# Kernel tuning notes

Hardware: AMD Instinct MI355X
Metric: run time of the kernel (lower is better)

## Reference

```python
import jax, jax.numpy as jnp
import numpy as np

P = 512       # input_shape
HD = 256      # hidden_dim
N = 65536     # number of samples
LAM1 = 1.0
LAM3 = 1.0


def setup_inputs() -> dict:
    key = jax.random.key(0)
    ks = jax.random.split(key, 12)
    def lin(kw, kb, out_d, in_d):
        lim = 1.0 / np.sqrt(in_d)
        W = jax.random.uniform(kw, (out_d, in_d), jnp.float32, -lim, lim)
        b = jax.random.uniform(kb, (out_d,), jnp.float32, -lim, lim)
        return W, b
    W1, b1 = lin(ks[0], ks[1], 200, P + HD)
    W12, b12 = lin(ks[2], ks[3], 100, 200)
    W13, b13 = lin(ks[4], ks[5], 100, 100)
    W2, b2 = lin(ks[6], ks[7], P, 100)
    return {
        "input": jax.random.normal(ks[8], (N, P), jnp.float32),
        "h": jax.random.normal(ks[9], (N, HD), jnp.float32),
        "W1": W1, "b1": b1, "W12": W12, "b12": b12,
        "W13": W13, "b13": b13, "W2": W2, "b2": b2,
        "idx0": 0, "idx1": N,
    }


def reference(input, h, W1, b1, W12, b12, W13, b13, W2, b2, idx0, idx1):
    n = input.shape[0]
    hs = h[idx0:idx1]                                   # [N, HD]
    x = jnp.concatenate([input, hs], axis=1)            # [N, P+HD]
    x = jax.nn.relu(x @ W1.T + b1)                      # dropout = identity (eval)
    x = jax.nn.relu(x @ W12.T + b12)
    x = jax.nn.relu(x @ W13.T + b13)
    f_x_h = x @ W2.T + b2                               # [N, P]
    mu = jnp.mean(hs, axis=0)                           # [HD]
    # S = mean_i <h_i, h_i> : vectorized sum-of-squares (replaces Python loop)
    S = jnp.mean(jnp.sum(hs * hs, axis=1))
    part0 = jnp.linalg.norm(f_x_h[:-1] - input[1:]) / (n - 1)
    part1 = LAM1 * jnp.sum(jnp.abs(mu)) / HD
    part2 = LAM1 * jnp.abs(S / HD - 1.0)
    part3 = LAM3 * jnp.mean(jnp.sum(jnp.abs(hs[1:] - hs[:-1]), axis=1)) / HD
    return (f_x_h, part0, part1, part2, part3)
```

## Files before the change

kernel.cpp:

```cpp
#include <hip/hip_runtime.h>

typedef __bf16 bf16;
typedef __bf16 bf16x8 __attribute__((ext_vector_type(8)));
typedef float f32x4 __attribute__((ext_vector_type(4)));

#define N_ROWS 65536

#define W1P_E  (208 * 768)
#define W12P_E (112 * 224)
#define W13P_E (112 * 128)
#define W2P_E  (512 * 128)
#define WP_TOTAL (W1P_E + W12P_E + W13P_E + W2P_E)
#define BP_OFF_BYTES (WP_TOTAL * 2)
#define BP_FLOATS 944
#define ACC_OFF_BYTES (BP_OFF_BYTES + BP_FLOATS * 4)
#define ACC_FLOATS 259

__global__ void pack_kernel(const float* __restrict__ W1, const float* __restrict__ b1,
                            const float* __restrict__ W12, const float* __restrict__ b12,
                            const float* __restrict__ W13, const float* __restrict__ b13,
                            const float* __restrict__ W2, const float* __restrict__ b2,
                            bf16* __restrict__ wp, float* __restrict__ bp) {
  int i = blockIdx.x * 256 + threadIdx.x;
  if (i < WP_TOTAL) {
    float v = 0.0f;
    if (i < W1P_E) {
      int o = i / 768, k = i - o * 768;
      if (o < 200) v = W1[o * 768 + k];
    } else if (i < W1P_E + W12P_E) {
      int j = i - W1P_E;
      int o = j / 224, k = j - o * 224;
      if (o < 100 && k < 200) v = W12[o * 200 + k];
    } else if (i < W1P_E + W12P_E + W13P_E) {
      int j = i - (W1P_E + W12P_E);
      int o = j / 128, k = j - o * 128;
      if (o < 100 && k < 100) v = W13[o * 100 + k];
    } else {
      int j = i - (W1P_E + W12P_E + W13P_E);
      int o = j / 128, k = j - o * 128;
      if (k < 100) v = W2[o * 100 + k];
    }
    wp[i] = (bf16)v;
  } else {
    int j = i - WP_TOTAL;
    if (j < BP_FLOATS) {
      float v = 0.0f;
      if (j < 208)      { if (j < 200) v = b1[j]; }
      else if (j < 320) { int o = j - 208; if (o < 100) v = b12[o]; }
      else if (j < 432) { int o = j - 320; if (o < 100) v = b13[o]; }
      else              { v = b2[j - 432]; }
      bp[j] = v;
    }
  }
}

__device__ inline bf16x8 cvt8(const float* __restrict__ p) {
  f32x4 lo = *(const f32x4*)p;
  f32x4 hi = *(const f32x4*)(p + 4);
  bf16x8 r;
#pragma unroll
  for (int i = 0; i < 4; i++) { r[i] = (bf16)lo[i]; r[4 + i] = (bf16)hi[i]; }
  return r;
}

#define MFMA(a, b, c) __builtin_amdgcn_mfma_f32_16x16x32_bf16((a), (b), (c), 0, 0, 0)

template<int ITERS, int R, int SRC_STRIDE>
__device__ inline void stage_load(bf16x8* r, const bf16* __restrict__ src, int k0, int tid) {
#pragma unroll
  for (int i = 0; i < ITERS; i++) {
    int e = tid + i * 256;
    if (ITERS * 256 == R * 4 || e < R * 4) {
      int row = e >> 2, seg = e & 3;
      r[i] = *(const bf16x8*)(src + (size_t)row * SRC_STRIDE + k0 + seg * 8);
    }
  }
}
template<int ITERS, int R>
__device__ inline void stage_write(bf16* dst, const bf16x8* r, int tid) {
#pragma unroll
  for (int i = 0; i < ITERS; i++) {
    int e = tid + i * 256;
    if (ITERS * 256 == R * 4 || e < R * 4) {
      int row = e >> 2, seg = e & 3;
      int ps = seg ^ ((row ^ (row >> 2)) & 3);
      *(bf16x8*)(dst + row * 32 + ps * 8) = r[i];
    }
  }
}

__global__ __launch_bounds__(256, 4) void mlp_main(
    const float* __restrict__ input, const float* __restrict__ h,
    const bf16* __restrict__ wp, const float* __restrict__ bp,
    float* __restrict__ out, float* __restrict__ p0_accum) {
  __shared__ __align__(16) bf16 acts[4][3712];
  __shared__ __align__(16) bf16 wbuf[2][6656];

  const int tid = threadIdx.x;
  const int lane = tid & 63;
  const int wave = tid >> 6;
  const int c16 = lane & 15;
  const int quad = lane >> 4;
  const int m0 = blockIdx.x * 64 + wave * 16;
  const int qs8 = (quad ^ ((c16 ^ (c16 >> 2)) & 3)) * 8;

  const bf16* W1p  = wp;
  const bf16* W12p = wp + W1P_E;
  const bf16* W13p = wp + W1P_E + W12P_E;
  const bf16* W2p  = wp + W1P_E + W12P_E + W13P_E;
  const float* b1p  = bp;
  const float* b12p = bp + 208;
  const float* b13p = bp + 320;
  const float* b2p  = bp + 432;

  bf16* actw = &acts[wave][0];
  bf16x8 sreg[4];

  f32x4 acc1[13];
#pragma unroll
  for (int t = 0; t < 13; t++) acc1[t] = (f32x4){0.f, 0.f, 0.f, 0.f};

  stage_load<4, 208, 768>(sreg, W1p, 0, tid);
  stage_write<4, 208>(wbuf[0], sreg, tid);
  __syncthreads();

  const float* arow = input + (size_t)(m0 + c16) * 512;
  const float* hrow = h + (size_t)(m0 + c16) * 256;
  for (int ks = 0; ks < 24; ks++) {
    if (ks + 1 < 24) stage_load<4, 208, 768>(sreg, W1p, (ks + 1) * 32, tid);
    const int k0 = ks * 32;
    bf16x8 a = (k0 < 512) ? cvt8(arow + k0 + quad * 8) : cvt8(hrow + (k0 - 512) + quad * 8);
    const bf16* buf = wbuf[ks & 1];
#pragma unroll
    for (int t = 0; t < 13; t++) {
      bf16x8 b = *(const bf16x8*)(buf + (t * 16 + c16) * 32 + qs8);
      acc1[t] = MFMA(a, b, acc1[t]);
    }
    if (ks + 1 < 24) stage_write<4, 208>(wbuf[(ks + 1) & 1], sreg, tid);
    __syncthreads();
  }
#pragma unroll
  for (int t = 0; t < 13; t++) {
    const float bias = b1p[t * 16 + c16];
#pragma unroll
    for (int r = 0; r < 4; r++)
      actw[(quad * 4 + r) * 232 + t * 16 + c16] = (bf16)fmaxf(acc1[t][r] + bias, 0.0f);
  }
  for (int idx = lane; idx < 256; idx += 64)
    actw[(idx >> 4) * 232 + 208 + (idx & 15)] = (bf16)0.0f;

  f32x4 acc2[7];
#pragma unroll
  for (int t = 0; t < 7; t++) acc2[t] = (f32x4){0.f, 0.f, 0.f, 0.f};

  stage_load<2, 112, 224>(sreg, W12p, 0, tid);
  stage_write<2, 112>(wbuf[0], sreg, tid);
  __syncthreads();
  for (int ks = 0; ks < 7; ks++) {
    if (ks + 1 < 7) stage_load<2, 112, 224>(sreg, W12p, (ks + 1) * 32, tid);
    const int k0 = ks * 32;
    bf16x8 a = *(const bf16x8*)(actw + c16 * 232 + k0 + quad * 8);
    const bf16* buf = wbuf[ks & 1];
#pragma unroll
    for (int t = 0; t < 7; t++) {
      bf16x8 b = *(const bf16x8*)(buf + (t * 16 + c16) * 32 + qs8);
      acc2[t] = MFMA(a, b, acc2[t]);
    }
    if (ks + 1 < 7) stage_write<2, 112>(wbuf[(ks + 1) & 1], sreg, tid);
    __syncthreads();
  }
#pragma unroll
  for (int t = 0; t < 7; t++) {
    const float bias = b12p[t * 16 + c16];
#pragma unroll
    for (int r = 0; r < 4; r++)
      actw[(quad * 4 + r) * 136 + t * 16 + c16] = (bf16)fmaxf(acc2[t][r] + bias, 0.0f);
  }
  for (int idx = lane; idx < 256; idx += 64)
    actw[(idx >> 4) * 136 + 112 + (idx & 15)] = (bf16)0.0f;

  f32x4 acc3[7];
#pragma unroll
  for (int t = 0; t < 7; t++) acc3[t] = (f32x4){0.f, 0.f, 0.f, 0.f};

  stage_load<2, 112, 128>(sreg, W13p, 0, tid);
  stage_write<2, 112>(wbuf[0], sreg, tid);
  __syncthreads();
  for (int ks = 0; ks < 4; ks++) {
    if (ks + 1 < 4) stage_load<2, 112, 128>(sreg, W13p, (ks + 1) * 32, tid);
    const int k0 = ks * 32;
    bf16x8 a = *(const bf16x8*)(actw + c16 * 136 + k0 + quad * 8);
    const bf16* buf = wbuf[ks & 1];
#pragma unroll
    for (int t = 0; t < 7; t++) {
      bf16x8 b = *(const bf16x8*)(buf + (t * 16 + c16) * 32 + qs8);
      acc3[t] = MFMA(a, b, acc3[t]);
    }
    if (ks + 1 < 4) stage_write<2, 112>(wbuf[(ks + 1) & 1], sreg, tid);
    __syncthreads();
  }
#pragma unroll
  for (int t = 0; t < 7; t++) {
    const float bias = b13p[t * 16 + c16];
#pragma unroll
    for (int r = 0; r < 4; r++)
      actw[(quad * 4 + r) * 136 + t * 16 + c16] = (bf16)fmaxf(acc3[t][r] + bias, 0.0f);
  }
  for (int idx = lane; idx < 256; idx += 64)
    actw[(idx >> 4) * 136 + 112 + (idx & 15)] = (bf16)0.0f;

  float p0local = 0.0f;
  for (int g = 0; g < 4; g++) {
    f32x4 acc4[8];
#pragma unroll
    for (int t = 0; t < 8; t++) acc4[t] = (f32x4){0.f, 0.f, 0.f, 0.f};

    const bf16* Wg = W2p + (size_t)g * 128 * 128;
    stage_load<2, 128, 128>(sreg, Wg, 0, tid);
    stage_write<2, 128>(wbuf[0], sreg, tid);
    __syncthreads();
    for (int ks = 0; ks < 4; ks++) {
      if (ks + 1 < 4) stage_load<2, 128, 128>(sreg, Wg, (ks + 1) * 32, tid);
      const int k0 = ks * 32;
      bf16x8 a = *(const bf16x8*)(actw + c16 * 136 + k0 + quad * 8);
      const bf16* buf = wbuf[ks & 1];
#pragma unroll
      for (int t = 0; t < 8; t++) {
        bf16x8 b = *(const bf16x8*)(buf + (t * 16 + c16) * 32 + qs8);
        acc4[t] = MFMA(a, b, acc4[t]);
      }
      if (ks + 1 < 4) stage_write<2, 128>(wbuf[(ks + 1) & 1], sreg, tid);
      __syncthreads();
    }
#pragma unroll
    for (int t = 0; t < 8; t++) {
      const int o = g * 128 + t * 16 + c16;
      const float bias = b2p[o];
#pragma unroll
      for (int r = 0; r < 4; r++) {
        const int grow = m0 + quad * 4 + r;
        float v = acc4[t][r] + bias;
        out[(size_t)grow * 512 + o] = v;
        if (grow < N_ROWS - 1) {
          float d = v - input[(size_t)(grow + 1) * 512 + o];
          p0local += d * d;
        }
      }
    }
  }
#pragma unroll
  for (int off = 32; off > 0; off >>= 1) p0local += __shfl_down(p0local, off);
  if (lane == 0) atomicAdd(p0_accum, p0local);
}

__global__ __launch_bounds__(256) void reduce_h(const float* __restrict__ h, float* __restrict__ acc) {
  __shared__ f32x4 cbuf[256];
  __shared__ float redS[256];
  __shared__ float redP[256];
  const int t = threadIdx.x;
  const int c = t & 63;
  const int rg = t >> 6;
  const int start = blockIdx.x * 128 + rg * 32;

  const float* base = h + (size_t)start * 256 + c * 4;
  f32x4 prev = *(const f32x4*)base;
  f32x4 csum = prev;
  f32x4 s2v = prev * prev;
  f32x4 p3v = (f32x4){0.f, 0.f, 0.f, 0.f};
#pragma unroll 8
  for (int r = 1; r < 32; r++) {
    f32x4 v = *(const f32x4*)(base + (size_t)r * 256);
    csum += v;
    s2v += v * v;
    f32x4 d = v - prev;
#pragma unroll
    for (int i = 0; i < 4; i++) p3v[i] += __builtin_fabsf(d[i]);
    prev = v;
  }
  if (start + 32 < N_ROWS) {
    f32x4 v = *(const f32x4*)(base + (size_t)32 * 256);
    f32x4 d = v - prev;
#pragma unroll
    for (int i = 0; i < 4; i++) p3v[i] += __builtin_fabsf(d[i]);
  }
  cbuf[t] = csum;
  redS[t] = s2v[0] + s2v[1] + s2v[2] + s2v[3];
  redP[t] = p3v[0] + p3v[1] + p3v[2] + p3v[3];
  __syncthreads();
  if (rg == 0) {
    f32x4 s = cbuf[c] + cbuf[c + 64] + cbuf[c + 128] + cbuf[c + 192];
    atomicAdd(&acc[4 * c + 0], s[0]);
    atomicAdd(&acc[4 * c + 1], s[1]);
    atomicAdd(&acc[4 * c + 2], s[2]);
    atomicAdd(&acc[4 * c + 3], s[3]);
  }
  for (int s = 128; s > 0; s >>= 1) {
    if (t < s) { redS[t] += redS[t + s]; redP[t] += redP[t + s]; }
    __syncthreads();
  }
  if (t == 0) {
    atomicAdd(&acc[257], redS[0]);
    atomicAdd(&acc[258], redP[0]);
  }
}

__global__ void finalize(const float* __restrict__ acc, float* __restrict__ out) {
  __shared__ float red[256];
  const int t = threadIdx.x;
  red[t] = fabsf(acc[t]);
  __syncthreads();
  for (int s = 128; s > 0; s >>= 1) {
    if (t < s) red[t] += red[t + s];
    __syncthreads();
  }
  if (t == 0) {
    float part1 = red[0] / 65536.0f / 256.0f;
    float part0 = sqrtf(acc[256]) / 65535.0f;
    float part2 = fabsf(acc[257] / (65536.0f * 256.0f) - 1.0f);
    float part3 = acc[258] / (65535.0f * 256.0f);
    out[(size_t)N_ROWS * 512 + 0] = part0;
    out[(size_t)N_ROWS * 512 + 1] = part1;
    out[(size_t)N_ROWS * 512 + 2] = part2;
    out[(size_t)N_ROWS * 512 + 3] = part3;
  }
}

extern "C" void kernel_launch(void* const* d_in, const int* in_sizes, int n_in,
                              void* d_out, int out_size, void* d_ws, size_t ws_size,
                              hipStream_t stream) {
  const float* input = (const float*)d_in[0];
  const float* h   = (const float*)d_in[1];
  const float* W1  = (const float*)d_in[2];
  const float* b1  = (const float*)d_in[3];
  const float* W12 = (const float*)d_in[4];
  const float* b12 = (const float*)d_in[5];
  const float* W13 = (const float*)d_in[6];
  const float* b13 = (const float*)d_in[7];
  const float* W2  = (const float*)d_in[8];
  const float* b2  = (const float*)d_in[9];
  float* out = (float*)d_out;

  bf16* wp = (bf16*)d_ws;
  float* bp = (float*)((char*)d_ws + BP_OFF_BYTES);
  float* acc = (float*)((char*)d_ws + ACC_OFF_BYTES);

  hipMemsetAsync(acc, 0, ACC_FLOATS * sizeof(float), stream);
  pack_kernel<<<(WP_TOTAL + BP_FLOATS + 255) / 256, 256, 0, stream>>>(
      W1, b1, W12, b12, W13, b13, W2, b2, wp, bp);
  mlp_main<<<N_ROWS / 64, 256, 0, stream>>>(input, h, wp, bp, out, acc + 256);
  reduce_h<<<N_ROWS / 128, 256, 0, stream>>>(h, acc);
  finalize<<<1, 256, 0, stream>>>(acc, out);
}
```

Baseline: 490.4 us.

## Pre-swizzle weight tiles and stage via direct global-to-LDS loads; batch activation loads

The pack kernel now writes weights in per-k-step, pre-swizzled tile order, so the main kernel can copy each stage straight into LDS with global_load_lds and skip the register round trip. Layer-1 activation loads are batched eight k-steps at a time to expose more memory parallelism, and launch bounds drop from 4 to 2 blocks per SM. The p0 atomic is reduced per block first, and reduce_h uses fewer, larger blocks spreading the column sums over 16 accumulator copies to cut atomic contention. Risks include lower occupancy, higher register pressure from the activation buffer, and reliance on the asynchronous LDS copies being complete at the barrier.

```diff
diff --git a/kernel.cpp b/kernel.cpp
--- a/kernel.cpp
+++ b/kernel.cpp
@@ -6,15 +6,24 @@
 
 #define N_ROWS 65536
 
-#define W1P_E  (208 * 768)
-#define W12P_E (112 * 224)
-#define W13P_E (112 * 128)
-#define W2P_E  (512 * 128)
-#define WP_TOTAL (W1P_E + W12P_E + W13P_E + W2P_E)
+#define W1_E   159744
+#define W12_E  25088
+#define W13_E  14336
+#define W2_E   65536
+#define WP_TOTAL (W1_E + W12_E + W13_E + W2_E)
+#define W12_OFF_B 319488
+#define W13_OFF_B 369664
+#define W2_OFF_B  398336
 #define BP_OFF_BYTES (WP_TOTAL * 2)
 #define BP_FLOATS 944
 #define ACC_OFF_BYTES (BP_OFF_BYTES + BP_FLOATS * 4)
-#define ACC_FLOATS 259
+#define NCOPY 16
+#define ACC_FLOATS (NCOPY * 256 + 3)
+#define P0_IDX (NCOPY * 256)
+#define S_IDX  (NCOPY * 256 + 1)
+#define P3_IDX (NCOPY * 256 + 2)
+
+__device__ inline int swz4(int r) { return (r ^ (r >> 2)) & 3; }
 
 __global__ void pack_kernel(const float* __restrict__ W1, const float* __restrict__ b1,
                             const float* __restrict__ W12, const float* __restrict__ b12,
@@ -24,20 +33,30 @@
   int i = blockIdx.x * 256 + threadIdx.x;
   if (i < WP_TOTAL) {
     float v = 0.0f;
-    if (i < W1P_E) {
-      int o = i / 768, k = i - o * 768;
-      if (o < 200) v = W1[o * 768 + k];
-    } else if (i < W1P_E + W12P_E) {
-      int j = i - W1P_E;
-      int o = j / 224, k = j - o * 224;
-      if (o < 100 && k < 200) v = W12[o * 200 + k];
-    } else if (i < W1P_E + W12P_E + W13P_E) {
-      int j = i - (W1P_E + W12P_E);
-      int o = j / 128, k = j - o * 128;
-      if (o < 100 && k < 100) v = W13[o * 100 + k];
+    if (i < W1_E) {
+      int s = i / 6656, b = i - s * 6656;
+      int r = b >> 5, w = b & 31;
+      int k = s * 32 + (((w >> 3) ^ swz4(r)) << 3) + (w & 7);
+      if (r < 200) v = W1[r * 768 + k];
+    } else if (i < W1_E + W12_E) {
+      int j = i - W1_E;
+      int s = j / 3584, b = j - s * 3584;
+      int r = b >> 5, w = b & 31;
+      int k = s * 32 + (((w >> 3) ^ swz4(r)) << 3) + (w & 7);
+      if (r < 100 && k < 200) v = W12[r * 200 + k];
+    } else if (i < W1_E + W12_E + W13_E) {
+      int j = i - (W1_E + W12_E);
+      int s = j / 3584, b = j - s * 3584;
+      int r = b >> 5, w = b & 31;
+      int k = s * 32 + (((w >> 3) ^ swz4(r)) << 3) + (w & 7);
+      if (r < 100 && k < 100) v = W13[r * 100 + k];
     } else {
-      int j = i - (W1P_E + W12P_E + W13P_E);
-      int o = j / 128, k = j - o * 128;
+      int j = i - (W1_E + W12_E + W13_E);
+      int g = j >> 14, rest = j & 16383;
+      int s = rest >> 12, b = rest & 4095;
+      int r = b >> 5, w = b & 31;
+      int o = g * 128 + r;
+      int k = s * 32 + (((w >> 3) ^ swz4(r)) << 3) + (w & 7);
       if (k < 100) v = W2[o * 100 + k];
     }
     wp[i] = (bf16)v;
@@ -54,47 +73,31 @@
   }
 }
 
-__device__ inline bf16x8 cvt8(const float* __restrict__ p) {
-  f32x4 lo = *(const f32x4*)p;
-  f32x4 hi = *(const f32x4*)(p + 4);
-  bf16x8 r;
-#pragma unroll
-  for (int i = 0; i < 4; i++) { r[i] = (bf16)lo[i]; r[4 + i] = (bf16)hi[i]; }
-  return r;
-}
-
 #define MFMA(a, b, c) __builtin_amdgcn_mfma_f32_16x16x32_bf16((a), (b), (c), 0, 0, 0)
 
-template<int ITERS, int R, int SRC_STRIDE>
-__device__ inline void stage_load(bf16x8* r, const bf16* __restrict__ src, int k0, int tid) {
-#pragma unroll
-  for (int i = 0; i < ITERS; i++) {
-    int e = tid + i * 256;
-    if (ITERS * 256 == R * 4 || e < R * 4) {
-      int row = e >> 2, seg = e & 3;
-      r[i] = *(const bf16x8*)(src + (size_t)row * SRC_STRIDE + k0 + seg * 8);
-    }
-  }
-}
-template<int ITERS, int R>
-__device__ inline void stage_write(bf16* dst, const bf16x8* r, int tid) {
-#pragma unroll
-  for (int i = 0; i < ITERS; i++) {
-    int e = tid + i * 256;
-    if (ITERS * 256 == R * 4 || e < R * 4) {
-      int row = e >> 2, seg = e & 3;
-      int ps = seg ^ ((row ^ (row >> 2)) & 3);
-      *(bf16x8*)(dst + row * 32 + ps * 8) = r[i];
-    }
-  }
-}
-
-__global__ __launch_bounds__(256, 4) void mlp_main(
+template<int BYTES>
+__device__ inline void stage(const char* __restrict__ src, bf16* __restrict__ dstw, int tid) {
+  char* dst = (char*)dstw;
+  const int off0 = (tid >> 6) * 1024 + (tid & 63) * 16;
+  constexpr int NCH = (BYTES + 4095) / 4096;
+#pragma unroll
+  for (int j = 0; j < NCH; j++) {
+    const int off = j * 4096 + off0;
+    if ((BYTES & 4095) == 0 || off < BYTES)
+      __builtin_amdgcn_global_load_lds(
+          (const __attribute__((address_space(1))) void*)(src + off),
+          (__attribute__((address_space(3))) void*)(dst + off),
+          16, 0, 0);
+  }
+}
+
+__global__ __launch_bounds__(256, 2) void mlp_main(
     const float* __restrict__ input, const float* __restrict__ h,
     const bf16* __restrict__ wp, const float* __restrict__ bp,
     float* __restrict__ out, float* __restrict__ p0_accum) {
   __shared__ __align__(16) bf16 acts[4][3712];
   __shared__ __align__(16) bf16 wbuf[2][6656];
+  __shared__ float p0red[4];
 
   const int tid = threadIdx.x;
   const int lane = tid & 63;
@@ -102,42 +105,49 @@
   const int c16 = lane & 15;
   const int quad = lane >> 4;
   const int m0 = blockIdx.x * 64 + wave * 16;
-  const int qs8 = (quad ^ ((c16 ^ (c16 >> 2)) & 3)) * 8;
-
-  const bf16* W1p  = wp;
-  const bf16* W12p = wp + W1P_E;
-  const bf16* W13p = wp + W1P_E + W12P_E;
-  const bf16* W2p  = wp + W1P_E + W12P_E + W13P_E;
+  const int qs8 = (quad ^ swz4(c16)) * 8;
+
+  const char* wpb = (const char*)wp;
   const float* b1p  = bp;
   const float* b12p = bp + 208;
   const float* b13p = bp + 320;
   const float* b2p  = bp + 432;
 
   bf16* actw = &acts[wave][0];
-  bf16x8 sreg[4];
 
   f32x4 acc1[13];
 #pragma unroll
   for (int t = 0; t < 13; t++) acc1[t] = (f32x4){0.f, 0.f, 0.f, 0.f};
 
-  stage_load<4, 208, 768>(sreg, W1p, 0, tid);
-  stage_write<4, 208>(wbuf[0], sreg, tid);
-  __syncthreads();
-
-  const float* arow = input + (size_t)(m0 + c16) * 512;
-  const float* hrow = h + (size_t)(m0 + c16) * 256;
-  for (int ks = 0; ks < 24; ks++) {
-    if (ks + 1 < 24) stage_load<4, 208, 768>(sreg, W1p, (ks + 1) * 32, tid);
-    const int k0 = ks * 32;
-    bf16x8 a = (k0 < 512) ? cvt8(arow + k0 + quad * 8) : cvt8(hrow + (k0 - 512) + quad * 8);
-    const bf16* buf = wbuf[ks & 1];
-#pragma unroll
-    for (int t = 0; t < 13; t++) {
-      bf16x8 b = *(const bf16x8*)(buf + (t * 16 + c16) * 32 + qs8);
-      acc1[t] = MFMA(a, b, acc1[t]);
-    }
-    if (ks + 1 < 24) stage_write<4, 208>(wbuf[(ks + 1) & 1], sreg, tid);
-    __syncthreads();
+  stage<13312>(wpb, wbuf[0], tid);
+  __syncthreads();
+
+  const float* arow = input + (size_t)(m0 + c16) * 512 + quad * 8;
+  const float* hrow = h + (size_t)(m0 + c16) * 256 + quad * 8;
+  f32x4 abuf[16];
+  for (int kb = 0; kb < 3; kb++) {
+#pragma unroll
+    for (int b = 0; b < 8; b++) {
+      const int kk = kb * 8 + b;
+      const float* p = (kk < 16) ? (arow + kk * 32) : (hrow + (kk - 16) * 32);
+      abuf[b * 2]     = *(const f32x4*)p;
+      abuf[b * 2 + 1] = *(const f32x4*)(p + 4);
+    }
+#pragma unroll
+    for (int b = 0; b < 8; b++) {
+      const int ks = kb * 8 + b;
+      if (ks + 1 < 24) stage<13312>(wpb + (ks + 1) * 13312, wbuf[(b + 1) & 1], tid);
+      bf16x8 a;
+#pragma unroll
+      for (int q = 0; q < 4; q++) { a[q] = (bf16)abuf[b * 2][q]; a[4 + q] = (bf16)abuf[b * 2 + 1][q]; }
+      const bf16* buf = wbuf[b & 1];
+#pragma unroll
+      for (int t = 0; t < 13; t++) {
+        bf16x8 bb = *(const bf16x8*)(buf + (t * 16 + c16) * 32 + qs8);
+        acc1[t] = MFMA(a, bb, acc1[t]);
+      }
+      __syncthreads();
+    }
   }
 #pragma unroll
   for (int t = 0; t < 13; t++) {
@@ -153,20 +163,18 @@
 #pragma unroll
   for (int t = 0; t < 7; t++) acc2[t] = (f32x4){0.f, 0.f, 0.f, 0.f};
 
-  stage_load<2, 112, 224>(sreg, W12p, 0, tid);
-  stage_write<2, 112>(wbuf[0], sreg, tid);
-  __syncthreads();
+  stage<7168>(wpb + W12_OFF_B, wbuf[0], tid);
+  __syncthreads();
+#pragma unroll
   for (int ks = 0; ks < 7; ks++) {
-    if (ks + 1 < 7) stage_load<2, 112, 224>(sreg, W12p, (ks + 1) * 32, tid);
-    const int k0 = ks * 32;
-    bf16x8 a = *(const bf16x8*)(actw + c16 * 232 + k0 + quad * 8);
+    if (ks + 1 < 7) stage<7168>(wpb + W12_OFF_B + (ks + 1) * 7168, wbuf[(ks + 1) & 1], tid);
+    bf16x8 a = *(const bf16x8*)(actw + c16 * 232 + ks * 32 + quad * 8);
     const bf16* buf = wbuf[ks & 1];
 #pragma unroll
     for (int t = 0; t < 7; t++) {
-      bf16x8 b = *(const bf16x8*)(buf + (t * 16 + c16) * 32 + qs8);
-      acc2[t] = MFMA(a, b, acc2[t]);
-    }
-    if (ks + 1 < 7) stage_write<2, 112>(wbuf[(ks + 1) & 1], sreg, tid);
+      bf16x8 bb = *(const bf16x8*)(buf + (t * 16 + c16) * 32 + qs8);
+      acc2[t] = MFMA(a, bb, acc2[t]);
+    }
     __syncthreads();
   }
 #pragma unroll
@@ -183,20 +191,18 @@
 #pragma unroll
   for (int t = 0; t < 7; t++) acc3[t] = (f32x4){0.f, 0.f, 0.f, 0.f};
 
-  stage_load<2, 112, 128>(sreg, W13p, 0, tid);
-  stage_write<2, 112>(wbuf[0], sreg, tid);
-  __syncthreads();
+  stage<7168>(wpb + W13_OFF_B, wbuf[0], tid);
+  __syncthreads();
+#pragma unroll
   for (int ks = 0; ks < 4; ks++) {
-    if (ks + 1 < 4) stage_load<2, 112, 128>(sreg, W13p, (ks + 1) * 32, tid);
-    const int k0 = ks * 32;
-    bf16x8 a = *(const bf16x8*)(actw + c16 * 136 + k0 + quad * 8);
+    if (ks + 1 < 4) stage<7168>(wpb + W13_OFF_B + (ks + 1) * 7168, wbuf[(ks + 1) & 1], tid);
+    bf16x8 a = *(const bf16x8*)(actw + c16 * 136 + ks * 32 + quad * 8);
     const bf16* buf = wbuf[ks & 1];
 #pragma unroll
     for (int t = 0; t < 7; t++) {
-      bf16x8 b = *(const bf16x8*)(buf + (t * 16 + c16) * 32 + qs8);
-      acc3[t] = MFMA(a, b, acc3[t]);
-    }
-    if (ks + 1 < 4) stage_write<2, 112>(wbuf[(ks + 1) & 1], sreg, tid);
+      bf16x8 bb = *(const bf16x8*)(buf + (t * 16 + c16) * 32 + qs8);
+      acc3[t] = MFMA(a, bb, acc3[t]);
+    }
     __syncthreads();
   }
 #pragma unroll
@@ -215,21 +221,19 @@
 #pragma unroll
     for (int t = 0; t < 8; t++) acc4[t] = (f32x4){0.f, 0.f, 0.f, 0.f};
 
-    const bf16* Wg = W2p + (size_t)g * 128 * 128;
-    stage_load<2, 128, 128>(sreg, Wg, 0, tid);
-    stage_write<2, 128>(wbuf[0], sreg, tid);
-    __syncthreads();
+    const char* Wg = wpb + W2_OFF_B + g * 32768;
+    stage<8192>(Wg, wbuf[0], tid);
+    __syncthreads();
+#pragma unroll
     for (int ks = 0; ks < 4; ks++) {
-      if (ks + 1 < 4) stage_load<2, 128, 128>(sreg, Wg, (ks + 1) * 32, tid);
-      const int k0 = ks * 32;
-      bf16x8 a = *(const bf16x8*)(actw + c16 * 136 + k0 + quad * 8);
+      if (ks + 1 < 4) stage<8192>(Wg + (ks + 1) * 8192, wbuf[(ks + 1) & 1], tid);
+      bf16x8 a = *(const bf16x8*)(actw + c16 * 136 + ks * 32 + quad * 8);
       const bf16* buf = wbuf[ks & 1];
 #pragma unroll
       for (int t = 0; t < 8; t++) {
-        bf16x8 b = *(const bf16x8*)(buf + (t * 16 + c16) * 32 + qs8);
-        acc4[t] = MFMA(a, b, acc4[t]);
+        bf16x8 bb = *(const bf16x8*)(buf + (t * 16 + c16) * 32 + qs8);
+        acc4[t] = MFMA(a, bb, acc4[t]);
       }
-      if (ks + 1 < 4) stage_write<2, 128>(wbuf[(ks + 1) & 1], sreg, tid);
       __syncthreads();
     }
 #pragma unroll
@@ -250,7 +254,9 @@
   }
 #pragma unroll
   for (int off = 32; off > 0; off >>= 1) p0local += __shfl_down(p0local, off);
-  if (lane == 0) atomicAdd(p0_accum, p0local);
+  if (lane == 0) p0red[wave] = p0local;
+  __syncthreads();
+  if (tid == 0) atomicAdd(p0_accum, p0red[0] + p0red[1] + p0red[2] + p0red[3]);
 }
 
 __global__ __launch_bounds__(256) void reduce_h(const float* __restrict__ h, float* __restrict__ acc) {
@@ -260,7 +266,7 @@
   const int t = threadIdx.x;
   const int c = t & 63;
   const int rg = t >> 6;
-  const int start = blockIdx.x * 128 + rg * 32;
+  const int start = blockIdx.x * 256 + rg * 64;
 
   const float* base = h + (size_t)start * 256 + c * 4;
   f32x4 prev = *(const f32x4*)base;
@@ -268,7 +274,7 @@
   f32x4 s2v = prev * prev;
   f32x4 p3v = (f32x4){0.f, 0.f, 0.f, 0.f};
 #pragma unroll 8
-  for (int r = 1; r < 32; r++) {
+  for (int r = 1; r < 64; r++) {
     f32x4 v = *(const f32x4*)(base + (size_t)r * 256);
     csum += v;
     s2v += v * v;
@@ -277,8 +283,8 @@
     for (int i = 0; i < 4; i++) p3v[i] += __builtin_fabsf(d[i]);
     prev = v;
   }
-  if (start + 32 < N_ROWS) {
-    f32x4 v = *(const f32x4*)(base + (size_t)32 * 256);
+  if (start + 64 < N_ROWS) {
+    f32x4 v = *(const f32x4*)(base + (size_t)64 * 256);
     f32x4 d = v - prev;
 #pragma unroll
     for (int i = 0; i < 4; i++) p3v[i] += __builtin_fabsf(d[i]);
@@ -289,39 +295,39 @@
   __syncthreads();
   if (rg == 0) {
     f32x4 s = cbuf[c] + cbuf[c + 64] + cbuf[c + 128] + cbuf[c + 192];
-    atomicAdd(&acc[4 * c + 0], s[0]);
-    atomicAdd(&acc[4 * c + 1], s[1]);
-    atomicAdd(&acc[4 * c + 2], s[2]);
-    atomicAdd(&acc[4 * c + 3], s[3]);
-  }
-  for (int s = 128; s > 0; s >>= 1) {
-    if (t < s) { redS[t] += redS[t + s]; redP[t] += redP[t + s]; }
+    float* dst = acc + (blockIdx.x & (NCOPY - 1)) * 256 + 4 * c;
+    atomicAdd(dst + 0, s[0]);
+    atomicAdd(dst + 1, s[1]);
+    atomicAdd(dst + 2, s[2]);
+    atomicAdd(dst + 3, s[3]);
+  }
+  for (int st = 128; st > 0; st >>= 1) {
+    if (t < st) { redS[t] += redS[t + st]; redP[t] += redP[t + st]; }
     __syncthreads();
   }
   if (t == 0) {
-    atomicAdd(&acc[257], redS[0]);
-    atomicAdd(&acc[258], redP[0]);
+    atomicAdd(&acc[S_IDX], redS[0]);
+    atomicAdd(&acc[P3_IDX], redP[0]);
   }
 }
 
 __global__ void finalize(const float* __restrict__ acc, float* __restrict__ out) {
   __shared__ float red[256];
   const int t = threadIdx.x;
-  red[t] = fabsf(acc[t]);
-  __syncthreads();
-  for (int s = 128; s > 0; s >>= 1) {
-    if (t < s) red[t] += red[t + s];
+  float s = 0.0f;
+#pragma unroll
+  for (int j = 0; j < NCOPY; j++) s += acc[j * 256 + t];
+  red[t] = fabsf(s);
+  __syncthreads();
+  for (int st = 128; st > 0; st >>= 1) {
+    if (t < st) red[t] += red[t + st];
     __syncthreads();
   }
   if (t == 0) {
-    float part1 = red[0] / 65536.0f / 256.0f;
-    float part0 = sqrtf(acc[256]) / 65535.0f;
-    float part2 = fabsf(acc[257] / (65536.0f * 256.0f) - 1.0f);
-    float part3 = acc[258] / (65535.0f * 256.0f);
-    out[(size_t)N_ROWS * 512 + 0] = part0;
-    out[(size_t)N_ROWS * 512 + 1] = part1;
-    out[(size_t)N_ROWS * 512 + 2] = part2;
-    out[(size_t)N_ROWS * 512 + 3] = part3;
+    out[(size_t)N_ROWS * 512 + 0] = sqrtf(acc[P0_IDX]) / 65535.0f;
+    out[(size_t)N_ROWS * 512 + 1] = red[0] / 65536.0f / 256.0f;
+    out[(size_t)N_ROWS * 512 + 2] = fabsf(acc[S_IDX] / (65536.0f * 256.0f) - 1.0f);
+    out[(size_t)N_ROWS * 512 + 3] = acc[P3_IDX] / (65535.0f * 256.0f);
   }
 }
 
@@ -347,7 +353,7 @@
   hipMemsetAsync(acc, 0, ACC_FLOATS * sizeof(float), stream);
   pack_kernel<<<(WP_TOTAL + BP_FLOATS + 255) / 256, 256, 0, stream>>>(
       W1, b1, W12, b12, W13, b13, W2, b2, wp, bp);
-  mlp_main<<<N_ROWS / 64, 256, 0, stream>>>(input, h, wp, bp, out, acc + 256);
-  reduce_h<<<N_ROWS / 128, 256, 0, stream>>>(h, acc);
+  mlp_main<<<N_ROWS / 64, 256, 0, stream>>>(input, h, wp, bp, out, acc + P0_IDX);
+  reduce_h<<<N_ROWS / 256, 256, 0, stream>>>(h, acc);
   finalize<<<1, 256, 0, stream>>>(acc, out);
 }
```

Result: faster. 412.9 us (-15.8%).
